# Kernel tuning notes

Hardware: AMD Instinct MI355X
Metric: run time of the kernel (lower is better)

Reference implementation:

```python
import jax, jax.numpy as jnp
import numpy as np
from jax import lax

B, C, H, W = 8, 256, 32, 32
HEADS = 8
NUM_OFF = 9
OFF_SCALE = 0.1


def setup_inputs() -> dict:
    key = jax.random.key(0)
    ks = jax.random.split(key, 8)
    f = lambda k, s, sc: jax.random.normal(k, s, dtype=jnp.float32) * sc
    return {
        'query_map': f(ks[0], (B, C, H, W), 1.0),
        'kv_map': f(ks[1], (B, C, H, W), 1.0),
        'Wq': f(ks[2], (C, C), C ** -0.5),
        'Wk': f(ks[3], (C, C), C ** -0.5),
        'Wv': f(ks[4], (C, C), C ** -0.5),
        'Woff1': f(ks[5], (C // 2, C, 3, 3), (C * 9) ** -0.5),
        'boff1': jnp.zeros((C // 2,), jnp.float32),
        'Woff2': f(ks[6], (NUM_OFF * 2, C // 2), (C // 2) ** -0.5),
        'boff2': jnp.zeros((NUM_OFF * 2,), jnp.float32),
        'Wout': f(ks[7], (C, C), C ** -0.5),
        'bout': jnp.zeros((C,), jnp.float32),
    }


def grid_sample_bilinear_border(img, grid):
    """img: (B,C,H,W); grid: (B,H,W,2) with (x,y) in [-1,1], align_corners=True,
    padding_mode='border'. Returns (B,C,H,W)."""
    Bn, Cn, Hn, Wn = img.shape
    x = (grid[..., 0] + 1.0) * 0.5 * (Wn - 1)
    y = (grid[..., 1] + 1.0) * 0.5 * (Hn - 1)
    # border padding: clamp continuous coords into the valid range
    x = jnp.clip(x, 0.0, Wn - 1)
    y = jnp.clip(y, 0.0, Hn - 1)
    x0 = jnp.floor(x)
    y0 = jnp.floor(y)
    wx = x - x0
    wy = y - y0
    x0i = x0.astype(jnp.int32)
    y0i = y0.astype(jnp.int32)
    x1i = jnp.minimum(x0i + 1, Wn - 1)
    y1i = jnp.minimum(y0i + 1, Hn - 1)
    flat = img.reshape(Bn, Cn, Hn * Wn)

    def gat(iy, ix):
        idx = (iy * Wn + ix).reshape(Bn, 1, -1)  # broadcasts over channels
        return jnp.take_along_axis(flat, idx, axis=2)

    v00 = gat(y0i, x0i)
    v01 = gat(y0i, x1i)
    v10 = gat(y1i, x0i)
    v11 = gat(y1i, x1i)
    wxf = wx.reshape(Bn, 1, -1)
    wyf = wy.reshape(Bn, 1, -1)
    out = (v00 * (1 - wxf) + v01 * wxf) * (1 - wyf) + (v10 * (1 - wxf) + v11 * wxf) * wyf
    return out.reshape(Bn, Cn, Hn, Wn)


def reference(query_map, kv_map, Wq, Wk, Wv, Woff1, boff1, Woff2, boff2, Wout, bout):
    Bn, Cn, Hn, Wn = query_map.shape
    hd = Cn // HEADS
    # 1x1 conv projections as channel einsums
    q = jnp.einsum('oc,bchw->bohw', Wq, query_map)
    # offset network: 3x3 conv -> relu -> 1x1 conv
    h1 = lax.conv_general_dilated(q, Woff1, (1, 1), 'SAME',
                                  dimension_numbers=('NCHW', 'OIHW', 'NCHW'))
    h1 = jax.nn.relu(h1 + boff1[None, :, None, None])
    offsets = jnp.einsum('oc,bchw->bohw', Woff2, h1) + boff2[None, :, None, None]
    offsets = offsets.reshape(Bn, NUM_OFF, 2, Hn, Wn)
    offset = offsets[:, 0] * OFF_SCALE  # (B,2,H,W); ch0 -> x, ch1 -> y
    # normalized base grid in [-1,1] (align_corners=True convention)
    gx = jnp.linspace(-1.0, 1.0, Wn, dtype=q.dtype)[None, :]  # (1,W)
    gy = jnp.linspace(-1.0, 1.0, Hn, dtype=q.dtype)[:, None]  # (H,1)
    vx = gx[None] + offset[:, 0]  # (B,H,W)
    vy = gy[None] + offset[:, 1]
    vgrid = jnp.stack([vx, vy], axis=-1)  # (B,H,W,2)
    kv_sampled = grid_sample_bilinear_border(kv_map, vgrid)
    k = jnp.einsum('oc,bchw->bohw', Wk, kv_sampled)
    v = jnp.einsum('oc,bchw->bohw', Wv, kv_sampled)
    # (B,C,H,W) -> (B,heads,HW,hd)
    def to_heads(t):
        return t.reshape(Bn, HEADS, hd, Hn * Wn).transpose(0, 1, 3, 2)
    qh, kh, vh = to_heads(q), to_heads(k), to_heads(v)
    scale = hd ** -0.5
    attn = jnp.einsum('bhqd,bhkd->bhqk', qh, kh) * scale
    attn = jax.nn.softmax(attn, axis=-1)
    out = jnp.einsum('bhqk,bhkd->bhqd', attn, vh)
    out = out.transpose(0, 1, 3, 2).reshape(Bn, Cn, Hn, Wn)
    out = jnp.einsum('oc,bchw->bohw', Wout, out) + bout[None, :, None, None]
    return out
```

## Files before the change

### kernel.cpp

```cpp
#include <hip/hip_runtime.h>

#define HW_ 1024

typedef __attribute__((ext_vector_type(8))) short bf16x8;
typedef __attribute__((ext_vector_type(4))) short bf16x4;
typedef __attribute__((ext_vector_type(4))) float f32x4;

__device__ inline unsigned short f2bf(float f) {
  unsigned int u = __float_as_uint(f);
  u += 0x7FFF + ((u >> 16) & 1);
  return (unsigned short)(u >> 16);
}
__device__ inline unsigned short f2bf_fast(float f) {
  return (unsigned short)((__float_as_uint(f) + 0x8000u) >> 16);
}
__device__ inline float bf2f(unsigned short h) {
  return __uint_as_float(((unsigned int)h) << 16);
}
__device__ inline void async_copy16(const void* g, void* l) {
  __builtin_amdgcn_global_load_lds(
      (const __attribute__((address_space(1))) unsigned int*)g,
      (__attribute__((address_space(3))) unsigned int*)l, 16, 0, 0);
}

__global__ __launch_bounds__(256) void fused0(
    const float* __restrict__ kv,
    const float* __restrict__ Wq, const float* __restrict__ Wk,
    const float* __restrict__ Wv, const float* __restrict__ Wo,
    const float* __restrict__ Woff1, const float* __restrict__ Xf,
    short* __restrict__ WH, short* __restrict__ WL, short* __restrict__ wb,
    float* __restrict__ kvT,
    short* __restrict__ Yt, short* __restrict__ Yh2, short* __restrict__ Yl2)
{
  __shared__ float T[256][33];
  __shared__ short Bsh[32][40];
  __shared__ short Bsl[32][40];
  const int bid = blockIdx.x, t = threadIdx.x;

  if (bid < 512) {
    const int w    = t >> 6;
    const int lane = t & 63;
    const int ln   = lane & 15;
    const int qd   = lane >> 4;
    const int bp0  = (bid & 255) * 32;
    const int om   = (bid >> 8) * 128 + w * 32;
    const int bB   = bp0 >> 10, p0l = bp0 & 1023;

    f32x4 acc[2][2] = {};
#pragma unroll
    for (int k0 = 0; k0 < 256; k0 += 32) {
      __syncthreads();
      {
        int pp = t & 31, cg = t >> 5;
        float fv[4];
#pragma unroll
        for (int j = 0; j < 4; ++j)
          fv[j] = Xf[((size_t)(bB * 256 + k0 + cg * 4 + j)) * HW_ + p0l + pp];
        bf16x4 h4, l4;
#pragma unroll
        for (int j = 0; j < 4; ++j) {
          unsigned short h = f2bf(fv[j]);
          h4[j] = (short)h;
          l4[j] = (short)f2bf(fv[j] - bf2f(h));
        }
        *(bf16x4*)&Bsh[pp][cg * 4] = h4;
        *(bf16x4*)&Bsl[pp][cg * 4] = l4;
      }
      __syncthreads();

      bf16x8 Ah[2], Al[2], Bh[2], Bl[2];
#pragma unroll
      for (int mt = 0; mt < 2; ++mt) {
        const float* ws = &Wq[((size_t)(om + mt * 16 + ln)) * 256 + k0 + qd * 8];
        float4 fa = *(const float4*)ws;
        float4 fb = *(const float4*)(ws + 4);
        float f8[8] = {fa.x, fa.y, fa.z, fa.w, fb.x, fb.y, fb.z, fb.w};
#pragma unroll
        for (int j = 0; j < 8; ++j) {
          unsigned short h = f2bf(f8[j]);
          Ah[mt][j] = (short)h;
          Al[mt][j] = (short)f2bf(f8[j] - bf2f(h));
        }
      }
#pragma unroll
      for (int nt = 0; nt < 2; ++nt) {
        Bh[nt] = *(const bf16x8*)&Bsh[nt * 16 + ln][qd * 8];
        Bl[nt] = *(const bf16x8*)&Bsl[nt * 16 + ln][qd * 8];
      }
#pragma unroll
      for (int mt = 0; mt < 2; ++mt)
#pragma unroll
        for (int nt = 0; nt < 2; ++nt) {
          acc[mt][nt] = __builtin_amdgcn_mfma_f32_16x16x32_bf16(Ah[mt], Bh[nt], acc[mt][nt], 0, 0, 0);
          acc[mt][nt] = __builtin_amdgcn_mfma_f32_16x16x32_bf16(Ah[mt], Bl[nt], acc[mt][nt], 0, 0, 0);
          acc[mt][nt] = __builtin_amdgcn_mfma_f32_16x16x32_bf16(Al[mt], Bh[nt], acc[mt][nt], 0, 0, 0);
        }
    }

    const float sc = 0.25506063286f;
#pragma unroll
    for (int mt = 0; mt < 2; ++mt)
#pragma unroll
      for (int nt = 0; nt < 2; ++nt) {
        int bp = bp0 + nt * 16 + ln;
        int b = bp >> 10, p = bp & 1023;
#pragma unroll
        for (int i = 0; i < 4; ++i) {
          int o = om + mt * 16 + qd * 4 + i;
          int h = o >> 5, d = o & 31;
          Yt[(((size_t)(b * 8 + h)) * 1024 + p) * 32 + d] = (short)f2bf(acc[mt][nt][i] * sc);
        }
        int ob = om + mt * 16 + qd * 4;
        bf16x4 h4, l4;
#pragma unroll
        for (int i = 0; i < 4; ++i) {
          float f = acc[mt][nt][i];
          unsigned short h = f2bf(f);
          h4[i] = (short)h;
          l4[i] = (short)f2bf(f - bf2f(h));
        }
        *(bf16x4*)&Yh2[(size_t)bp * 256 + ob] = h4;
        *(bf16x4*)&Yl2[(size_t)bp * 256 + ob] = l4;
      }

  } else if (bid < 768) {
    int tb = bid - 512;
    int b = tb >> 5, p0 = (tb & 31) * 32;
    int pp = t & 31, cg = t >> 5;
#pragma unroll
    for (int i = 0; i < 32; ++i) {
      int c = cg * 32 + i;
      T[c][pp] = kv[((size_t)(b * 256 + c)) * HW_ + p0 + pp];
    }
    __syncthreads();
#pragma unroll
    for (int r = 0; r < 8; ++r) {
      int e = t + 256 * r;
      int c4 = (e & 63) * 4, pp2 = e >> 6;
      float4 v4;
      v4.x = T[c4 + 0][pp2];
      v4.y = T[c4 + 1][pp2];
      v4.z = T[c4 + 2][pp2];
      v4.w = T[c4 + 3][pp2];
      *(float4*)&kvT[((size_t)(b * 1024 + p0 + pp2)) * 256 + c4] = v4;
    }
  } else if (bid < 960) {
    int b2 = bid - 768;
    int mat = b2 >> 6;
    int loc = (b2 & 63) * 1024 + t * 4;
    const float* W = (mat == 0) ? Wk : (mat == 1) ? Wv : Wo;
    float4 f4 = *(const float4*)&W[loc];
    float f[4] = {f4.x, f4.y, f4.z, f4.w};
    bf16x4 h4, l4;
#pragma unroll
    for (int j = 0; j < 4; ++j) {
      unsigned short h = f2bf(f[j]);
      h4[j] = (short)h;
      l4[j] = (short)f2bf(f[j] - bf2f(h));
    }
    if (mat == 2) {
      *(bf16x4*)&WH[3 * 65536 + loc] = h4;
      *(bf16x4*)&WL[3 * 65536 + loc] = l4;
    } else {
      int r = loc >> 8, c = loc & 255;
      int mtile = r >> 4, k0s = c >> 5;
      int lane_ = ((c >> 3) & 3) * 16 + (r & 15);
      int pidx = (((mtile * 8 + k0s) * 64 + lane_) * 8) + (c & 7);
      *(bf16x4*)&WH[(mat + 1) * 65536 + pidx] = h4;
      *(bf16x4*)&WL[(mat + 1) * 65536 + pidx] = l4;
    }
  } else {
    int e0 = (bid - 960) * 1024 + t * 4;
    int c = e0 & 255;
    int o = (e0 >> 8) & 127;
    int tap = e0 >> 15;
    bf16x4 h4;
#pragma unroll
    for (int j = 0; j < 4; ++j)
      h4[j] = (short)f2bf(Woff1[((size_t)(o * 256 + c + j)) * 9 + tap]);
    int otile = o >> 4, c0s = c >> 5;
    int lane_ = ((c >> 3) & 3) * 16 + (o & 15);
    int widx = ((((tap * 8 + otile) * 8 + c0s) * 64 + lane_) * 8) + (c & 7);
    *(bf16x4*)&wb[widx] = h4;
  }
}

__global__ __launch_bounds__(512) void convkv(
    const short* __restrict__ wb, const float* __restrict__ bias,
    const float* __restrict__ W2, const float* __restrict__ b2,
    const short* __restrict__ xh, const short* __restrict__ xl,
    const float* __restrict__ kvT,
    const short* __restrict__ WH, const short* __restrict__ WL,
    short* __restrict__ kt, short* __restrict__ vt)
{
  __shared__ short Xs[2][3][34][264];
  __shared__ short XsH[32][264];
  __shared__ short XsL[32][264];
  __shared__ float red[4][32][2];
  __shared__ float2 crd[32];
  const int id   = blockIdx.x;
  const int b    = id & 7;
  const int y0   = id >> 3;
  const int t    = threadIdx.x;
  const int w    = t >> 6;
  const int lane = t & 63;
  const int ln   = lane & 15;
  const int qd   = lane >> 4;
  const int bp0  = (b * 32 + y0) * 32;

  {
    bf16x8 v[12];
#pragma unroll
    for (int i = 0; i < 12; ++i) {
      int e = t + 512 * i;
      int oct = e & 31;
      int x   = (e >> 5) & 31;
      int rr  = e >> 10;
      int hl  = rr / 3, r = rr % 3;
      int yy  = y0 + r - 1;
      bf16x8 val = {};
      if (yy >= 0 && yy < 32) {
        const short* src = hl ? xl : xh;
        val = *(const bf16x8*)&src[((size_t)((b * 32 + yy) * 32 + x)) * 256 + oct * 8];
      }
      v[i] = val;
    }
#pragma unroll
    for (int i = 0; i < 12; ++i) {
      int e = t + 512 * i;
      int oct = e & 31;
      int x   = (e >> 5) & 31;
      int rr  = e >> 10;
      int hl  = rr / 3, r = rr % 3;
      *(bf16x8*)&Xs[hl][r][x + 1][oct * 8] = v[i];
    }
    if (t < 384) {
      int oct  = t & 31;
      int colw = (t >> 5) & 1;
      int rr   = t >> 6;
      int hl   = rr / 3, r = rr % 3;
      bf16x8 zz = {};
      *(bf16x8*)&Xs[hl][r][colw ? 33 : 0][oct * 8] = zz;
    }
  }
  __syncthreads();

  const int chh = w >> 2;
  const int ow  = w & 3;
  const int o0c = ow * 32;
  f32x4 acc[2][2] = {};
#pragma unroll
  for (int c0s = 0; c0s < 4; ++c0s) {
    const int c0 = chh * 128 + c0s * 32;
    const int c0abs = chh * 4 + c0s;
#pragma unroll
    for (int tap = 0; tap < 9; ++tap) {
      const int ky = tap / 3, kx = tap % 3;
      bf16x8 afr[2];
#pragma unroll
      for (int m = 0; m < 2; ++m)
        afr[m] = *(const bf16x8*)&wb[((((tap * 8 + (ow * 2 + m)) * 8 + c0abs) * 64
                                       + lane) * 8)];
#pragma unroll
      for (int nt = 0; nt < 2; ++nt) {
        int hc = nt * 16 + ln + kx;
        bf16x8 bh = *(const bf16x8*)&Xs[0][ky][hc][c0 + qd * 8];
        bf16x8 bl = *(const bf16x8*)&Xs[1][ky][hc][c0 + qd * 8];
#pragma unroll
        for (int m = 0; m < 2; ++m) {
          acc[m][nt] = __builtin_amdgcn_mfma_f32_16x16x32_bf16(afr[m], bh, acc[m][nt], 0, 0, 0);
          acc[m][nt] = __builtin_amdgcn_mfma_f32_16x16x32_bf16(afr[m], bl, acc[m][nt], 0, 0, 0);
        }
      }
    }
  }

  float* ps = (float*)&XsH[0][0];
  if (w >= 4) {
#pragma unroll
    for (int m = 0; m < 2; ++m)
#pragma unroll
      for (int nt = 0; nt < 2; ++nt)
        *(f32x4*)&ps[(((w - 4) * 64 + lane) * 4 + m * 2 + nt) * 4] = acc[m][nt];
  }
  __syncthreads();

  if (w < 4) {
    float ps0[2] = {0.f, 0.f}, ps1[2] = {0.f, 0.f};
#pragma unroll
    for (int m = 0; m < 2; ++m)
#pragma unroll
      for (int nt = 0; nt < 2; ++nt) {
        f32x4 p = *(const f32x4*)&ps[((w * 64 + lane) * 4 + m * 2 + nt) * 4];
        acc[m][nt] += p;
      }
#pragma unroll
    for (int m = 0; m < 2; ++m)
#pragma unroll
      for (int i = 0; i < 4; ++i) {
        int o = o0c + m * 16 + qd * 4 + i;
        float bo = bias[o];
        float w2a = W2[o], w2b = W2[128 + o];
#pragma unroll
        for (int nt = 0; nt < 2; ++nt) {
          float h = fmaxf(acc[m][nt][i] + bo, 0.f);
          ps0[nt] += w2a * h;
          ps1[nt] += w2b * h;
        }
      }
#pragma unroll
    for (int msk = 16; msk < 64; msk <<= 1) {
      ps0[0] += __shfl_xor(ps0[0], msk, 64);
      ps0[1] += __shfl_xor(ps0[1], msk, 64);
      ps1[0] += __shfl_xor(ps1[0], msk, 64);
      ps1[1] += __shfl_xor(ps1[1], msk, 64);
    }
    if (qd == 0) {
#pragma unroll
      for (int nt = 0; nt < 2; ++nt) {
        red[w][nt * 16 + ln][0] = ps0[nt];
        red[w][nt * 16 + ln][1] = ps1[nt];
      }
    }
  }
  __syncthreads();
  if (t < 32) {
    float c0s = (red[0][t][0] + red[1][t][0]) + (red[2][t][0] + red[3][t][0]) + b2[0];
    float c1s = (red[0][t][1] + red[1][t][1]) + (red[2][t][1] + red[3][t][1]) + b2[1];
    float gx = -1.f + 2.f * (float)t / 31.f;
    float gy = -1.f + 2.f * (float)y0 / 31.f;
    float vx = gx + 0.1f * c0s;
    float vy = gy + 0.1f * c1s;
    float px = fminf(fmaxf((vx + 1.f) * 0.5f * 31.f, 0.f), 31.f);
    float py = fminf(fmaxf((vy + 1.f) * 0.5f * 31.f, 0.f), 31.f);
    crd[t] = make_float2(px, py);
  }
  __syncthreads();

#pragma unroll
  for (int it = 0; it < 2; ++it) {
    int e = t + 512 * it;
    int oct = e & 31, row = e >> 5;
    float2 cd = crd[row];
    float x0f = floorf(cd.x), y0f = floorf(cd.y);
    float wx = cd.x - x0f, wy = cd.y - y0f;
    int x0 = (int)x0f, y0i = (int)y0f;
    int x1 = min(x0 + 1, 31), y1 = min(y0i + 1, 31);
    float w00 = (1.f - wx) * (1.f - wy), w01 = wx * (1.f - wy);
    float w10 = (1.f - wx) * wy,         w11 = wx * wy;
    const float* r00 = &kvT[((size_t)(b * 1024 + y0i * 32 + x0)) * 256 + oct * 8];
    const float* r01 = &kvT[((size_t)(b * 1024 + y0i * 32 + x1)) * 256 + oct * 8];
    const float* r10 = &kvT[((size_t)(b * 1024 + y1 * 32 + x0)) * 256 + oct * 8];
    const float* r11 = &kvT[((size_t)(b * 1024 + y1 * 32 + x1)) * 256 + oct * 8];
    float4 a00 = *(const float4*)r00, b00 = *(const float4*)(r00 + 4);
    float4 a01 = *(const float4*)r01, b01 = *(const float4*)(r01 + 4);
    float4 a10 = *(const float4*)r10, b10 = *(const float4*)(r10 + 4);
    float4 a11 = *(const float4*)r11, b11 = *(const float4*)(r11 + 4);
    float v[8];
    v[0] = a00.x * w00 + a01.x * w01 + a10.x * w10 + a11.x * w11;
    v[1] = a00.y * w00 + a01.y * w01 + a10.y * w10 + a11.y * w11;
    v[2] = a00.z * w00 + a01.z * w01 + a10.z * w10 + a11.z * w11;
    v[3] = a00.w * w00 + a01.w * w01 + a10.w * w10 + a11.w * w11;
    v[4] = b00.x * w00 + b01.x * w01 + b10.x * w10 + b11.x * w11;
    v[5] = b00.y * w00 + b01.y * w01 + b10.y * w10 + b11.y * w11;
    v[6] = b00.z * w00 + b01.z * w01 + b10.z * w10 + b11.z * w11;
    v[7] = b00.w * w00 + b01.w * w01 + b10.w * w10 + b11.w * w11;
    bf16x8 h8, l8;
#pragma unroll
    for (int j = 0; j < 8; ++j) {
      unsigned short h = f2bf(v[j]);
      h8[j] = (short)h;
      l8[j] = (short)f2bf(v[j] - bf2f(h));
    }
    *(bf16x8*)&XsH[row][oct * 8] = h8;
    *(bf16x8*)&XsL[row][oct * 8] = l8;
  }
  __syncthreads();

  const int mat  = w >> 2;
  const short* WAh = WH + (mat ? 131072 : 65536);
  const short* WAl = WL + (mat ? 131072 : 65536);
  const int om4 = (w & 3) * 4;

  f32x4 acg[4][2] = {};
#pragma unroll
  for (int k0 = 0; k0 < 256; k0 += 32) {
    const int k0s = k0 >> 5;
    bf16x8 Bh[2], Bl[2];
#pragma unroll
    for (int nt = 0; nt < 2; ++nt) {
      Bh[nt] = *(const bf16x8*)&XsH[nt * 16 + ln][k0 + qd * 8];
      Bl[nt] = *(const bf16x8*)&XsL[nt * 16 + ln][k0 + qd * 8];
    }
#pragma unroll
    for (int mt = 0; mt < 4; ++mt) {
      size_t wi = ((size_t)(((om4 + mt) * 8 + k0s) * 64 + lane)) * 8;
      bf16x8 Ah = *(const bf16x8*)&WAh[wi];
      bf16x8 Al = *(const bf16x8*)&WAl[wi];
#pragma unroll
      for (int nt = 0; nt < 2; ++nt) {
        acg[mt][nt] = __builtin_amdgcn_mfma_f32_16x16x32_bf16(Ah, Bh[nt], acg[mt][nt], 0, 0, 0);
        acg[mt][nt] = __builtin_amdgcn_mfma_f32_16x16x32_bf16(Ah, Bl[nt], acg[mt][nt], 0, 0, 0);
        acg[mt][nt] = __builtin_amdgcn_mfma_f32_16x16x32_bf16(Al, Bh[nt], acg[mt][nt], 0, 0, 0);
      }
    }
  }

#pragma unroll
  for (int mt = 0; mt < 4; ++mt)
#pragma unroll
    for (int nt = 0; nt < 2; ++nt) {
      int p  = bp0 + nt * 16 + ln;
      int pl = p & 1023;
      int jt = pl >> 6, jl = pl & 63;
#pragma unroll
      for (int i = 0; i < 4; ++i) {
        int oc = (w & 3) * 64 + mt * 16 + qd * 4 + i;
        unsigned short val = f2bf(acg[mt][nt][i]);
        int bhead = b * 8 + (oc >> 5), d = oc & 31;
        if (mat == 0) {
          int cd2 = (d >> 3) ^ ((jl >> 2) & 3);
          kt[((((size_t)(bhead * 16 + jt)) * 64 + jl) * 4 + cd2) * 8 + (d & 7)] = (short)val;
        } else {
          int jjs = ((jl & 15) << 2) | (jl >> 4);
          int cj = (jjs >> 3) ^ (d & 7);
          vt[((((size_t)(bhead * 16 + jt)) * 32 + d) * 8 + cj) * 8 + (jjs & 7)] = (short)val;
        }
      }
    }
}

__global__ __launch_bounds__(256) void attn_mfma(
    const short* __restrict__ qt, const short* __restrict__ kt,
    const short* __restrict__ vt, short* __restrict__ aoh,
    short* __restrict__ aol)
{
  __shared__ __align__(16) short Ks[2][2048];
  __shared__ __align__(16) short Vs[2][2048];
  __shared__ __align__(16) short P[4][32][72];
  const int t    = threadIdx.x;
  const int w    = t >> 6;
  const int lane = t & 63;
  const int ln   = lane & 15;
  const int qd   = lane >> 4;
  const int id   = blockIdx.x;
  const int b    = id & 7;
  const int rem  = id >> 3;
  const int h    = rem & 7;
  const int qc   = rem >> 3;
  const int bh   = b * 8 + h;
  const int qbase = qc * 128 + w * 16;

  const short* ktb = kt + (size_t)bh * 32768;
  const short* vtb = vt + (size_t)bh * 32768;

  bf16x8 aq[2];
  aq[0] = *(const bf16x8*)&qt[((size_t)(bh * 1024 + qbase + ln)) * 32 + qd * 8];
  aq[1] = *(const bf16x8*)&qt[((size_t)(bh * 1024 + qbase + 64 + ln)) * 32 + qd * 8];

  f32x4 acc[2][2] = {};
  float lacc[2][4] = {};
  const f32x4 zero = {0.f, 0.f, 0.f, 0.f};

  const int stoff = w * 512 + lane * 8;
  const int ldoff = w * 512;

  async_copy16(&ktb[stoff], &Ks[0][ldoff]);
  async_copy16(&vtb[stoff], &Vs[0][ldoff]);
  __syncthreads();

  for (int jt = 0; jt < 16; ++jt) {
    const int cur = jt & 1, nxt = cur ^ 1;
    if (jt < 15) {
      async_copy16(&ktb[(jt + 1) * 2048 + stoff], &Ks[nxt][ldoff]);
      async_copy16(&vtb[(jt + 1) * 2048 + stoff], &Vs[nxt][ldoff]);
    }

    bf16x8 bk[4], bv[2][2];
#pragma unroll
    for (int kk = 0; kk < 4; ++kk)
      bk[kk] = *(const bf16x8*)&Ks[cur][((kk * 16 + ln) * 4 + (qd ^ ((ln >> 2) & 3))) * 8];
#pragma unroll
    for (int kc = 0; kc < 2; ++kc)
#pragma unroll
      for (int ds = 0; ds < 2; ++ds)
        bv[kc][ds] = *(const bf16x8*)&Vs[cur][((ds * 16 + ln) * 8 + ((kc * 4 + qd) ^ (ln & 7))) * 8];

#pragma unroll
    for (int qf = 0; qf < 2; ++qf) {
      f32x4 s[4];
      __builtin_amdgcn_s_setprio(1);
#pragma unroll
      for (int kk = 0; kk < 4; ++kk)
        s[kk] = __builtin_amdgcn_mfma_f32_16x16x32_bf16(aq[qf], bk[kk], zero, 0, 0, 0);
      __builtin_amdgcn_s_setprio(0);

#pragma unroll
      for (int i = 0; i < 4; ++i) {
        float p0 = __builtin_amdgcn_exp2f(s[0][i]);
        float p1 = __builtin_amdgcn_exp2f(s[1][i]);
        float p2 = __builtin_amdgcn_exp2f(s[2][i]);
        float p3 = __builtin_amdgcn_exp2f(s[3][i]);
        s[0][i] = p0; s[1][i] = p1; s[2][i] = p2; s[3][i] = p3;
        lacc[qf][i] += (p0 + p1) + (p2 + p3);
      }
#pragma unroll
      for (int i = 0; i < 4; ++i) {
        bf16x4 p4;
#pragma unroll
        for (int kk = 0; kk < 4; ++kk) p4[kk] = (short)f2bf_fast(s[kk][i]);
        *(bf16x4*)&P[w][qf * 16 + qd * 4 + i][4 * ln] = p4;
      }
      __builtin_amdgcn_s_setprio(1);
#pragma unroll
      for (int kc = 0; kc < 2; ++kc) {
        bf16x8 ap = *(const bf16x8*)&P[w][qf * 16 + ln][kc * 32 + qd * 8];
#pragma unroll
        for (int ds = 0; ds < 2; ++ds)
          acc[qf][ds] = __builtin_amdgcn_mfma_f32_16x16x32_bf16(ap, bv[kc][ds], acc[qf][ds], 0, 0, 0);
      }
      __builtin_amdgcn_s_setprio(0);
    }

    __syncthreads();
  }

  const int bb = bh >> 3, hh2 = bh & 7;
#pragma unroll
  for (int qf = 0; qf < 2; ++qf)
#pragma unroll
    for (int i = 0; i < 4; ++i) {
      float l = lacc[qf][i];
      l += __shfl_xor(l, 1, 64);
      l += __shfl_xor(l, 2, 64);
      l += __shfl_xor(l, 4, 64);
      l += __shfl_xor(l, 8, 64);
      float inv = 1.f / l;
      int qrow = qbase + qf * 64 + qd * 4 + i;
#pragma unroll
      for (int ds = 0; ds < 2; ++ds) {
        float v = acc[qf][ds][i] * inv;
        unsigned short hv = f2bf(v);
        size_t idx = ((size_t)(bb * 1024 + qrow)) * 256 + hh2 * 32 + ds * 16 + ln;
        aoh[idx] = (short)hv;
        aol[idx] = (short)f2bf(v - bf2f(hv));
      }
    }
}

__global__ __launch_bounds__(256) void gemm_out(
    const short* __restrict__ Wh, const short* __restrict__ Wl,
    const short* __restrict__ Xh, const short* __restrict__ Xl,
    const float* __restrict__ bias, float* __restrict__ Yf)
{
  const int t    = threadIdx.x;
  const int w    = t >> 6;
  const int lane = t & 63;
  const int ln   = lane & 15;
  const int qd   = lane >> 4;
  const int bp0  = blockIdx.x * 32;
  const int om   = blockIdx.y * 128 + w * 32;

  f32x4 acc[2][2] = {};
#pragma unroll
  for (int k0 = 0; k0 < 256; k0 += 32) {
    bf16x8 Ah[2], Al[2], Bh[2], Bl[2];
#pragma unroll
    for (int mt = 0; mt < 2; ++mt) {
      size_t wi = ((size_t)(om + mt * 16 + ln)) * 256 + k0 + qd * 8;
      Ah[mt] = *(const bf16x8*)&Wh[wi];
      Al[mt] = *(const bf16x8*)&Wl[wi];
    }
#pragma unroll
    for (int nt = 0; nt < 2; ++nt) {
      size_t xi = ((size_t)(bp0 + nt * 16 + ln)) * 256 + k0 + qd * 8;
      Bh[nt] = *(const bf16x8*)&Xh[xi];
      Bl[nt] = *(const bf16x8*)&Xl[xi];
    }
#pragma unroll
    for (int mt = 0; mt < 2; ++mt)
#pragma unroll
      for (int nt = 0; nt < 2; ++nt) {
        acc[mt][nt] = __builtin_amdgcn_mfma_f32_16x16x32_bf16(Ah[mt], Bh[nt], acc[mt][nt], 0, 0, 0);
        acc[mt][nt] = __builtin_amdgcn_mfma_f32_16x16x32_bf16(Ah[mt], Bl[nt], acc[mt][nt], 0, 0, 0);
        acc[mt][nt] = __builtin_amdgcn_mfma_f32_16x16x32_bf16(Al[mt], Bh[nt], acc[mt][nt], 0, 0, 0);
      }
  }

#pragma unroll
  for (int mt = 0; mt < 2; ++mt)
#pragma unroll
    for (int i = 0; i < 4; ++i) {
      int o = om + mt * 16 + qd * 4 + i;
      float bo = bias[o];
#pragma unroll
      for (int nt = 0; nt < 2; ++nt) {
        int bp = bp0 + nt * 16 + ln;
        int b = bp >> 10, p = bp & 1023;
        Yf[((size_t)(b * 256 + o)) * HW_ + p] = acc[mt][nt][i] + bo;
      }
    }
}

extern "C" void kernel_launch(void* const* d_in, const int* in_sizes, int n_in,
                              void* d_out, int out_size, void* d_ws, size_t ws_size,
                              hipStream_t stream)
{
  const float* query_map = (const float*)d_in[0];
  const float* kv_map    = (const float*)d_in[1];
  const float* Wq        = (const float*)d_in[2];
  const float* Wk        = (const float*)d_in[3];
  const float* Wv        = (const float*)d_in[4];
  const float* Woff1     = (const float*)d_in[5];
  const float* boff1     = (const float*)d_in[6];
  const float* Woff2     = (const float*)d_in[7];
  const float* boff2     = (const float*)d_in[8];
  const float* Wout      = (const float*)d_in[9];
  const float* bout      = (const float*)d_in[10];
  float* out = (float*)d_out;
  char* base = (char*)d_ws;

  const size_t MB = 1u << 20;
  short* qt     = (short*)(base + 1 * MB);
  short* kt     = (short*)(base + 5 * MB);
  short* vt     = (short*)(base + 9 * MB);
  short* bufBh  = (short*)(base + 13 * MB);
  short* bufBl  = (short*)(base + 17 * MB);
  short* wb     = (short*)(base + 21 * MB);
  short* WH     = (short*)(base + 22 * MB);
  short* WL     = (short*)(base + 23 * MB);
  float* kvT    = (float*)(base + 24 * MB);

  fused0<<<dim3(1248), dim3(256), 0, stream>>>(kv_map, Wq, Wk, Wv, Wout, Woff1,
                                               query_map, WH, WL, wb, kvT,
                                               qt, bufBh, bufBl);
  convkv<<<dim3(256), dim3(512), 0, stream>>>(wb, boff1, Woff2, boff2,
                                              bufBh, bufBl, kvT, WH, WL, kt, vt);
  attn_mfma<<<dim3(512), dim3(256), 0, stream>>>(qt, kt, vt, bufBh, bufBl);
  gemm_out<<<dim3(256, 2), dim3(256), 0, stream>>>(WH + 196608, WL + 196608,
                                                   bufBh, bufBl, bout, out);
}
```

Measured before the change: 171.0 us.

## Split Q projection into its own kernel using pre-packed bf16 weights

The Q projection GEMM moves out of the fused prep kernel into a separate qgemm kernel. Wq is now converted once into the MFMA-packed hi/lo bf16 layout, so GEMM blocks no longer each re-convert fp32 weights. The output-projection weights also switch to the packed layout. gemm_out now stages its activation tile in shared memory before the K loop instead of reading it from global memory in every wave. The cost is an extra kernel launch and a serial dependency between the prep and Q-GEMM stages.

```diff
diff --git a/kernel.cpp b/kernel.cpp
--- a/kernel.cpp
+++ b/kernel.cpp
@@ -23,109 +23,19 @@
       (__attribute__((address_space(3))) unsigned int*)l, 16, 0, 0);
 }
 
-__global__ __launch_bounds__(256) void fused0(
+__global__ __launch_bounds__(256) void prep(
     const float* __restrict__ kv,
     const float* __restrict__ Wq, const float* __restrict__ Wk,
     const float* __restrict__ Wv, const float* __restrict__ Wo,
-    const float* __restrict__ Woff1, const float* __restrict__ Xf,
+    const float* __restrict__ Woff1,
     short* __restrict__ WH, short* __restrict__ WL, short* __restrict__ wb,
-    float* __restrict__ kvT,
-    short* __restrict__ Yt, short* __restrict__ Yh2, short* __restrict__ Yl2)
+    float* __restrict__ kvT)
 {
   __shared__ float T[256][33];
-  __shared__ short Bsh[32][40];
-  __shared__ short Bsl[32][40];
   const int bid = blockIdx.x, t = threadIdx.x;
 
-  if (bid < 512) {
-    const int w    = t >> 6;
-    const int lane = t & 63;
-    const int ln   = lane & 15;
-    const int qd   = lane >> 4;
-    const int bp0  = (bid & 255) * 32;
-    const int om   = (bid >> 8) * 128 + w * 32;
-    const int bB   = bp0 >> 10, p0l = bp0 & 1023;
-
-    f32x4 acc[2][2] = {};
-#pragma unroll
-    for (int k0 = 0; k0 < 256; k0 += 32) {
-      __syncthreads();
-      {
-        int pp = t & 31, cg = t >> 5;
-        float fv[4];
-#pragma unroll
-        for (int j = 0; j < 4; ++j)
-          fv[j] = Xf[((size_t)(bB * 256 + k0 + cg * 4 + j)) * HW_ + p0l + pp];
-        bf16x4 h4, l4;
-#pragma unroll
-        for (int j = 0; j < 4; ++j) {
-          unsigned short h = f2bf(fv[j]);
-          h4[j] = (short)h;
-          l4[j] = (short)f2bf(fv[j] - bf2f(h));
-        }
-        *(bf16x4*)&Bsh[pp][cg * 4] = h4;
-        *(bf16x4*)&Bsl[pp][cg * 4] = l4;
-      }
-      __syncthreads();
-
-      bf16x8 Ah[2], Al[2], Bh[2], Bl[2];
-#pragma unroll
-      for (int mt = 0; mt < 2; ++mt) {
-        const float* ws = &Wq[((size_t)(om + mt * 16 + ln)) * 256 + k0 + qd * 8];
-        float4 fa = *(const float4*)ws;
-        float4 fb = *(const float4*)(ws + 4);
-        float f8[8] = {fa.x, fa.y, fa.z, fa.w, fb.x, fb.y, fb.z, fb.w};
-#pragma unroll
-        for (int j = 0; j < 8; ++j) {
-          unsigned short h = f2bf(f8[j]);
-          Ah[mt][j] = (short)h;
-          Al[mt][j] = (short)f2bf(f8[j] - bf2f(h));
-        }
-      }
-#pragma unroll
-      for (int nt = 0; nt < 2; ++nt) {
-        Bh[nt] = *(const bf16x8*)&Bsh[nt * 16 + ln][qd * 8];
-        Bl[nt] = *(const bf16x8*)&Bsl[nt * 16 + ln][qd * 8];
-      }
-#pragma unroll
-      for (int mt = 0; mt < 2; ++mt)
-#pragma unroll
-        for (int nt = 0; nt < 2; ++nt) {
-          acc[mt][nt] = __builtin_amdgcn_mfma_f32_16x16x32_bf16(Ah[mt], Bh[nt], acc[mt][nt], 0, 0, 0);
-          acc[mt][nt] = __builtin_amdgcn_mfma_f32_16x16x32_bf16(Ah[mt], Bl[nt], acc[mt][nt], 0, 0, 0);
-          acc[mt][nt] = __builtin_amdgcn_mfma_f32_16x16x32_bf16(Al[mt], Bh[nt], acc[mt][nt], 0, 0, 0);
-        }
-    }
-
-    const float sc = 0.25506063286f;
-#pragma unroll
-    for (int mt = 0; mt < 2; ++mt)
-#pragma unroll
-      for (int nt = 0; nt < 2; ++nt) {
-        int bp = bp0 + nt * 16 + ln;
-        int b = bp >> 10, p = bp & 1023;
-#pragma unroll
-        for (int i = 0; i < 4; ++i) {
-          int o = om + mt * 16 + qd * 4 + i;
-          int h = o >> 5, d = o & 31;
-          Yt[(((size_t)(b * 8 + h)) * 1024 + p) * 32 + d] = (short)f2bf(acc[mt][nt][i] * sc);
-        }
-        int ob = om + mt * 16 + qd * 4;
-        bf16x4 h4, l4;
-#pragma unroll
-        for (int i = 0; i < 4; ++i) {
-          float f = acc[mt][nt][i];
-          unsigned short h = f2bf(f);
-          h4[i] = (short)h;
-          l4[i] = (short)f2bf(f - bf2f(h));
-        }
-        *(bf16x4*)&Yh2[(size_t)bp * 256 + ob] = h4;
-        *(bf16x4*)&Yl2[(size_t)bp * 256 + ob] = l4;
-      }
-
-  } else if (bid < 768) {
-    int tb = bid - 512;
-    int b = tb >> 5, p0 = (tb & 31) * 32;
+  if (bid < 256) {
+    int b = bid >> 5, p0 = (bid & 31) * 32;
     int pp = t & 31, cg = t >> 5;
 #pragma unroll
     for (int i = 0; i < 32; ++i) {
@@ -144,11 +54,11 @@
       v4.w = T[c4 + 3][pp2];
       *(float4*)&kvT[((size_t)(b * 1024 + p0 + pp2)) * 256 + c4] = v4;
     }
-  } else if (bid < 960) {
-    int b2 = bid - 768;
+  } else if (bid < 512) {
+    int b2 = bid - 256;
     int mat = b2 >> 6;
     int loc = (b2 & 63) * 1024 + t * 4;
-    const float* W = (mat == 0) ? Wk : (mat == 1) ? Wv : Wo;
+    const float* W = (mat == 0) ? Wq : (mat == 1) ? Wk : (mat == 2) ? Wv : Wo;
     float4 f4 = *(const float4*)&W[loc];
     float f[4] = {f4.x, f4.y, f4.z, f4.w};
     bf16x4 h4, l4;
@@ -158,19 +68,14 @@
       h4[j] = (short)h;
       l4[j] = (short)f2bf(f[j] - bf2f(h));
     }
-    if (mat == 2) {
-      *(bf16x4*)&WH[3 * 65536 + loc] = h4;
-      *(bf16x4*)&WL[3 * 65536 + loc] = l4;
-    } else {
-      int r = loc >> 8, c = loc & 255;
-      int mtile = r >> 4, k0s = c >> 5;
-      int lane_ = ((c >> 3) & 3) * 16 + (r & 15);
-      int pidx = (((mtile * 8 + k0s) * 64 + lane_) * 8) + (c & 7);
-      *(bf16x4*)&WH[(mat + 1) * 65536 + pidx] = h4;
-      *(bf16x4*)&WL[(mat + 1) * 65536 + pidx] = l4;
-    }
+    int r = loc >> 8, c = loc & 255;
+    int mtile = r >> 4, k0s = c >> 5;
+    int lane_ = ((c >> 3) & 3) * 16 + (r & 15);
+    int pidx = (((mtile * 8 + k0s) * 64 + lane_) * 8) + (c & 7);
+    *(bf16x4*)&WH[mat * 65536 + pidx] = h4;
+    *(bf16x4*)&WL[mat * 65536 + pidx] = l4;
   } else {
-    int e0 = (bid - 960) * 1024 + t * 4;
+    int e0 = (bid - 512) * 1024 + t * 4;
     int c = e0 & 255;
     int o = (e0 >> 8) & 127;
     int tap = e0 >> 15;
@@ -183,6 +88,95 @@
     int widx = ((((tap * 8 + otile) * 8 + c0s) * 64 + lane_) * 8) + (c & 7);
     *(bf16x4*)&wb[widx] = h4;
   }
+}
+
+__global__ __launch_bounds__(256) void qgemm(
+    const short* __restrict__ WH, const short* __restrict__ WL,
+    const float* __restrict__ Xf,
+    short* __restrict__ Yt, short* __restrict__ Yh2, short* __restrict__ Yl2)
+{
+  __shared__ short Bsh[32][40];
+  __shared__ short Bsl[32][40];
+  const int t    = threadIdx.x;
+  const int w    = t >> 6;
+  const int lane = t & 63;
+  const int ln   = lane & 15;
+  const int qd   = lane >> 4;
+  const int bp0  = blockIdx.x * 32;
+  const int mb   = blockIdx.y * 8 + w * 2;
+  const int bB   = bp0 >> 10, p0l = bp0 & 1023;
+
+  f32x4 acc[2][2] = {};
+#pragma unroll
+  for (int k0 = 0; k0 < 256; k0 += 32) {
+    __syncthreads();
+    {
+      int pp = t & 31, cg = t >> 5;
+      float fv[4];
+#pragma unroll
+      for (int j = 0; j < 4; ++j)
+        fv[j] = Xf[((size_t)(bB * 256 + k0 + cg * 4 + j)) * HW_ + p0l + pp];
+      bf16x4 h4, l4;
+#pragma unroll
+      for (int j = 0; j < 4; ++j) {
+        unsigned short h = f2bf(fv[j]);
+        h4[j] = (short)h;
+        l4[j] = (short)f2bf(fv[j] - bf2f(h));
+      }
+      *(bf16x4*)&Bsh[pp][cg * 4] = h4;
+      *(bf16x4*)&Bsl[pp][cg * 4] = l4;
+    }
+    __syncthreads();
+
+    bf16x8 Ah[2], Al[2], Bh[2], Bl[2];
+    const int k0s = k0 >> 5;
+#pragma unroll
+    for (int mt = 0; mt < 2; ++mt) {
+      size_t wi = ((size_t)(((mb + mt) * 8 + k0s) * 64 + lane)) * 8;
+      Ah[mt] = *(const bf16x8*)&WH[wi];
+      Al[mt] = *(const bf16x8*)&WL[wi];
+    }
+#pragma unroll
+    for (int nt = 0; nt < 2; ++nt) {
+      Bh[nt] = *(const bf16x8*)&Bsh[nt * 16 + ln][qd * 8];
+      Bl[nt] = *(const bf16x8*)&Bsl[nt * 16 + ln][qd * 8];
+    }
+#pragma unroll
+    for (int mt = 0; mt < 2; ++mt)
+#pragma unroll
+      for (int nt = 0; nt < 2; ++nt) {
+        acc[mt][nt] = __builtin_amdgcn_mfma_f32_16x16x32_bf16(Ah[mt], Bh[nt], acc[mt][nt], 0, 0, 0);
+        acc[mt][nt] = __builtin_amdgcn_mfma_f32_16x16x32_bf16(Ah[mt], Bl[nt], acc[mt][nt], 0, 0, 0);
+        acc[mt][nt] = __builtin_amdgcn_mfma_f32_16x16x32_bf16(Al[mt], Bh[nt], acc[mt][nt], 0, 0, 0);
+      }
+  }
+
+  const int om = blockIdx.y * 128 + w * 32;
+  const float sc = 0.25506063286f;
+#pragma unroll
+  for (int mt = 0; mt < 2; ++mt)
+#pragma unroll
+    for (int nt = 0; nt < 2; ++nt) {
+      int bp = bp0 + nt * 16 + ln;
+      int b = bp >> 10, p = bp & 1023;
+#pragma unroll
+      for (int i = 0; i < 4; ++i) {
+        int o = om + mt * 16 + qd * 4 + i;
+        int h = o >> 5, d = o & 31;
+        Yt[(((size_t)(b * 8 + h)) * 1024 + p) * 32 + d] = (short)f2bf(acc[mt][nt][i] * sc);
+      }
+      int ob = om + mt * 16 + qd * 4;
+      bf16x4 h4, l4;
+#pragma unroll
+      for (int i = 0; i < 4; ++i) {
+        float f = acc[mt][nt][i];
+        unsigned short h = f2bf(f);
+        h4[i] = (short)h;
+        l4[i] = (short)f2bf(f - bf2f(h));
+      }
+      *(bf16x4*)&Yh2[(size_t)bp * 256 + ob] = h4;
+      *(bf16x4*)&Yl2[(size_t)bp * 256 + ob] = l4;
+    }
 }
 
 __global__ __launch_bounds__(512) void convkv(
@@ -553,29 +547,42 @@
     const short* __restrict__ Xh, const short* __restrict__ Xl,
     const float* __restrict__ bias, float* __restrict__ Yf)
 {
+  __shared__ short XsH[32][264];
+  __shared__ short XsL[32][264];
   const int t    = threadIdx.x;
   const int w    = t >> 6;
   const int lane = t & 63;
   const int ln   = lane & 15;
   const int qd   = lane >> 4;
   const int bp0  = blockIdx.x * 32;
-  const int om   = blockIdx.y * 128 + w * 32;
+  const int mb   = blockIdx.y * 8 + w * 2;
+
+#pragma unroll
+  for (int it = 0; it < 4; ++it) {
+    int e = t + 256 * it;
+    int oct = e & 31, row = e >> 5;
+    bf16x8 vh = *(const bf16x8*)&Xh[((size_t)(bp0 + row)) * 256 + oct * 8];
+    bf16x8 vl = *(const bf16x8*)&Xl[((size_t)(bp0 + row)) * 256 + oct * 8];
+    *(bf16x8*)&XsH[row][oct * 8] = vh;
+    *(bf16x8*)&XsL[row][oct * 8] = vl;
+  }
+  __syncthreads();
 
   f32x4 acc[2][2] = {};
 #pragma unroll
   for (int k0 = 0; k0 < 256; k0 += 32) {
+    const int k0s = k0 >> 5;
     bf16x8 Ah[2], Al[2], Bh[2], Bl[2];
 #pragma unroll
     for (int mt = 0; mt < 2; ++mt) {
-      size_t wi = ((size_t)(om + mt * 16 + ln)) * 256 + k0 + qd * 8;
+      size_t wi = ((size_t)(((mb + mt) * 8 + k0s) * 64 + lane)) * 8;
       Ah[mt] = *(const bf16x8*)&Wh[wi];
       Al[mt] = *(const bf16x8*)&Wl[wi];
     }
 #pragma unroll
     for (int nt = 0; nt < 2; ++nt) {
-      size_t xi = ((size_t)(bp0 + nt * 16 + ln)) * 256 + k0 + qd * 8;
-      Bh[nt] = *(const bf16x8*)&Xh[xi];
-      Bl[nt] = *(const bf16x8*)&Xl[xi];
+      Bh[nt] = *(const bf16x8*)&XsH[nt * 16 + ln][k0 + qd * 8];
+      Bl[nt] = *(const bf16x8*)&XsL[nt * 16 + ln][k0 + qd * 8];
     }
 #pragma unroll
     for (int mt = 0; mt < 2; ++mt)
@@ -587,6 +594,7 @@
       }
   }
 
+  const int om = blockIdx.y * 128 + w * 32;
 #pragma unroll
   for (int mt = 0; mt < 2; ++mt)
 #pragma unroll
@@ -631,9 +639,10 @@
   short* WL     = (short*)(base + 23 * MB);
   float* kvT    = (float*)(base + 24 * MB);
 
-  fused0<<<dim3(1248), dim3(256), 0, stream>>>(kv_map, Wq, Wk, Wv, Wout, Woff1,
-                                               query_map, WH, WL, wb, kvT,
-                                               qt, bufBh, bufBl);
+  prep<<<dim3(800), dim3(256), 0, stream>>>(kv_map, Wq, Wk, Wv, Wout, Woff1,
+                                            WH, WL, wb, kvT);
+  qgemm<<<dim3(256, 2), dim3(256), 0, stream>>>(WH, WL, query_map,
+                                                qt, bufBh, bufBl);
   convkv<<<dim3(256), dim3(512), 0, stream>>>(wb, boff1, Woff2, boff2,
                                               bufBh, bufBl, kvT, WH, WL, kt, vt);
   attn_mfma<<<dim3(512), dim3(256), 0, stream>>>(qt, kt, vt, bufBh, bufBl);
```

Result: faster. 161.9 us (-5.3%).
